# Optimization experiments

Hardware: AMD Instinct MI355X
Metric: run time of the kernel (lower is better)

## Reference

```python
import jax, jax.numpy as jnp
import numpy as np

N = 100000        # nodes
E = 3200000       # edges
IN = 256          # in_feats
H = 8             # num_heads
O = 64            # out_feats
F = 64            # edge_feats
T = 8             # num_etypes

def setup_inputs() -> dict:
    key = jax.random.key(0)
    ks = jax.random.split(key, 10)
    return {
        "feat": jax.random.normal(ks[0], (N, IN), jnp.float32) * 0.1,
        "etype": jax.random.randint(ks[1], (E,), 0, T, jnp.int32),
        "src": jax.random.randint(ks[2], (E,), 0, N, jnp.int32),
        "dst": jax.random.randint(ks[3], (E,), 0, N, jnp.int32),
        "W_fc": jax.random.normal(ks[4], (IN, H * O), jnp.float32) * (1.0 / np.sqrt(IN)),
        "edge_emb": jax.random.normal(ks[5], (T, F), jnp.float32),
        "W_e": jax.random.normal(ks[6], (F, H * F), jnp.float32) * (1.0 / np.sqrt(F)),
        "attn_l": jax.random.normal(ks[7], (H, O), jnp.float32) * 0.1,
        "attn_r": jax.random.normal(ks[8], (H, O), jnp.float32) * 0.1,
        "attn_e": jax.random.normal(ks[9], (H, F), jnp.float32) * 0.1,
    }

def reference(feat, etype, src, dst, W_fc, edge_emb, W_e, attn_l, attn_r, attn_e):
    n = feat.shape[0]
    # node projection + per-head attention logits
    h = (feat @ W_fc).reshape(n, H, O)                      # [N,H,O]
    el = jnp.einsum('nho,ho->nh', h, attn_l)                # [N,H]
    er = jnp.einsum('nho,ho->nh', h, attn_r)                # [N,H]
    # edge-type embedding -> projection -> logit (project the tiny table once, then gather)
    emb_proj = (edge_emb @ W_e).reshape(T, H, F)            # [T,H,F]
    ee = jnp.einsum('thf,hf->th', emb_proj, attn_e)[etype]  # [E,H]
    # u_add_v + edge bias, then ReLU (module's "leaky_relu" is nn.ReLU())
    e = jax.nn.relu(el[src] + er[dst] + ee)                 # [E,H]
    # segment softmax grouped by destination node
    m = jax.ops.segment_max(e, dst, num_segments=n)         # [N,H]
    ex = jnp.exp(e - m[dst])                                # [E,H]
    s = jax.ops.segment_sum(ex, dst, num_segments=n)        # [N,H]
    return ex / s[dst]                                      # [E,H]
```

## Files before the change

kernel.cpp:

```cpp
#include <hip/hip_runtime.h>
#include <math.h>

#define NN 100000
#define NE 3200000
#define INF_ 256
#define NH 8
#define OF 64
#define EF 64
#define NT 8

#define BSH 7
#define BNODES 128
#define NB 782
#define CAPB 4608
#define SPLIT 4
#define EPB 4096

static constexpr size_t WS_AT      = 0;
static constexpr size_t WS_EE      = 4096;
static constexpr size_t WS_EL      = 4160;
static constexpr size_t WS_ERS     = WS_EL + (size_t)NN * 8;
static constexpr size_t WS_CCNT    = WS_ERS + (size_t)NN * 16;
static constexpr size_t WS_PART    = WS_CCNT + NB + 2;

__global__ __launch_bounds__(256) void k_prep_A(const float* __restrict__ W_fc,
                                                const float* __restrict__ attn_l,
                                                const float* __restrict__ attn_r,
                                                float* __restrict__ At,
                                                unsigned* __restrict__ ccnt) {
    int t = blockIdx.x * 256 + threadIdx.x;
    if (t < NB) ccnt[t] = 0u;
    int c = t >> 8;
    int i = t & 255;
    int h = c & 7;
    const float* attn = (c < 8) ? attn_l : attn_r;
    const float* wrow = W_fc + (size_t)i * (NH * OF) + h * OF;
    const float* arow = attn + h * OF;
    float acc = 0.f;
#pragma unroll 8
    for (int o = 0; o < OF; ++o) acc += wrow[o] * arow[o];
    At[c * INF_ + i] = acc;
}

__global__ __launch_bounds__(512) void k_prep_ee(const float* __restrict__ edge_emb,
                                                 const float* __restrict__ W_e,
                                                 const float* __restrict__ attn_e,
                                                 float* __restrict__ ee_tab) {
    __shared__ float B[EF][NH];
    int t = threadIdx.x;
    int g = t >> 3, h = t & 7;
    const float* wrow = W_e + (size_t)g * (NH * EF) + h * EF;
    const float* arow = attn_e + h * EF;
    float acc = 0.f;
#pragma unroll 8
    for (int f = 0; f < EF; ++f) acc += wrow[f] * arow[f];
    B[g][h] = acc;
    __syncthreads();
    if (t < NT * NH) {
        int tt = t >> 3, hh = t & 7;
        float a = 0.f;
#pragma unroll 8
        for (int g2 = 0; g2 < EF; ++g2) a += edge_emb[tt * EF + g2] * B[g2][hh];
        ee_tab[tt * NH + hh] = a;
    }
}

__global__ __launch_bounds__(256) void k_node(const float* __restrict__ feat,
                                              const float* __restrict__ At,
                                              float* __restrict__ el,
                                              float* __restrict__ ers) {
    int n = blockIdx.x * 256 + threadIdx.x;
    if (n >= NN) return;
    const float4* f4 = (const float4*)(feat + (size_t)n * INF_);
    const float4* A4 = (const float4*)At;
    float acc[16];
#pragma unroll
    for (int c = 0; c < 16; ++c) acc[c] = 0.f;
    for (int iq = 0; iq < INF_ / 4; ++iq) {
        float4 f = f4[iq];
#pragma unroll
        for (int c = 0; c < 16; ++c) {
            float4 a = A4[c * 64 + iq];
            acc[c] += f.x * a.x + f.y * a.y + f.z * a.z + f.w * a.w;
        }
    }
    float4* e4 = (float4*)(el + (size_t)n * 8);
    e4[0] = make_float4(acc[0], acc[1], acc[2], acc[3]);
    e4[1] = make_float4(acc[4], acc[5], acc[6], acc[7]);
    float4* r4 = (float4*)(ers + (size_t)n * 16);
    r4[0] = make_float4(acc[8], acc[9], acc[10], acc[11]);
    r4[1] = make_float4(acc[12], acc[13], acc[14], acc[15]);
    r4[2] = make_float4(0.f, 0.f, 0.f, 0.f);
    r4[3] = make_float4(0.f, 0.f, 0.f, 0.f);
}

__global__ __launch_bounds__(256) void k_partition(const int* __restrict__ src,
                                                   const int* __restrict__ dst,
                                                   const int* __restrict__ etype,
                                                   unsigned* __restrict__ ccnt,
                                                   unsigned* __restrict__ part) {
    __shared__ unsigned hist[NB];
    __shared__ unsigned cursor[NB];
    int tid = threadIdx.x;
    size_t base = (size_t)blockIdx.x * EPB;
    unsigned long long rc[16];
    for (int i = tid; i < NB; i += 256) hist[i] = 0u;
    __syncthreads();
#pragma unroll
    for (int k = 0; k < 16; ++k) {
        size_t j = base + (size_t)k * 256 + tid;
        if (j < NE) {
            int dj = dst[j];
            rc[k] = (unsigned long long)(unsigned)src[j]
                  | ((unsigned long long)(unsigned)etype[j] << 17)
                  | ((unsigned long long)(unsigned)dj << 20);
            atomicAdd(&hist[dj >> BSH], 1u);
        } else rc[k] = ~0ull;
    }
    __syncthreads();
    for (int i = tid; i < NB; i += 256) {
        unsigned h = hist[i];
        cursor[i] = h ? atomicAdd(ccnt + i, h) : 0u;
    }
    __syncthreads();
#pragma unroll
    for (int k = 0; k < 16; ++k) {
        if (rc[k] == ~0ull) continue;
        int dj = (int)(rc[k] >> 20);
        int b = dj >> BSH;
        unsigned pos = atomicAdd(&cursor[b], 1u);
        if (pos < CAPB)
            part[(size_t)b * CAPB + pos] =
                (unsigned)(rc[k] & 0xFFFFFull) | ((unsigned)(dj & (BNODES - 1)) << 20);
    }
}

__global__ __launch_bounds__(256) void k_bucket_sum(const unsigned* __restrict__ part,
                                                    const unsigned* __restrict__ ccnt,
                                                    const float* __restrict__ el,
                                                    const float* __restrict__ ers,
                                                    const float* __restrict__ ee_tab,
                                                    float* __restrict__ ers_out) {
    __shared__ float sbin[BNODES * 9];
    int bs = blockIdx.x;
    int b = bs >> 2, c = bs & 3;
    int tid = threadIdx.x;
    int n0 = b << BSH;
    int nn = NN - n0; if (nn > BNODES) nn = BNODES;

    for (int i = tid; i < BNODES * 9; i += 256) sbin[i] = 0.f;
    __syncthreads();

    unsigned cnt = ccnt[b]; if (cnt > CAPB) cnt = CAPB;
    const unsigned* pp = part + (size_t)b * CAPB;
    for (unsigned e = (unsigned)(c * 256 + tid); e < cnt; e += 1024) {
        unsigned rec = pp[e];
        int sj = (int)(rec & 0x1FFFFu);
        int et = (int)((rec >> 17) & 7u);
        int dl = (int)((rec >> 20) & (BNODES - 1));
        const float4* el4 = (const float4*)(el + (size_t)sj * 8);
        const float4* E   = (const float4*)(ers + (size_t)(n0 + dl) * 16);
        const float4* ee4 = (const float4*)(ee_tab + et * NH);
        float4 la = el4[0], lb = el4[1];
        float4 ra = E[0],   rb = E[1];
        float4 ea = ee4[0], eb = ee4[1];
        float* sb = &sbin[dl * 9];
        atomicAdd(&sb[0], __expf(fmaxf(la.x + ra.x + ea.x, 0.f)));
        atomicAdd(&sb[1], __expf(fmaxf(la.y + ra.y + ea.y, 0.f)));
        atomicAdd(&sb[2], __expf(fmaxf(la.z + ra.z + ea.z, 0.f)));
        atomicAdd(&sb[3], __expf(fmaxf(la.w + ra.w + ea.w, 0.f)));
        atomicAdd(&sb[4], __expf(fmaxf(lb.x + rb.x + eb.x, 0.f)));
        atomicAdd(&sb[5], __expf(fmaxf(lb.y + rb.y + eb.y, 0.f)));
        atomicAdd(&sb[6], __expf(fmaxf(lb.z + rb.z + eb.z, 0.f)));
        atomicAdd(&sb[7], __expf(fmaxf(lb.w + rb.w + eb.w, 0.f)));
    }
    __syncthreads();
    for (int i = tid; i < nn * NH; i += 256) {
        int nl = i >> 3, hh = i & 7;
        atomicAdd(&ers_out[(size_t)(n0 + nl) * 16 + 8 + hh], sbin[nl * 9 + hh]);
    }
}

__global__ __launch_bounds__(256) void k_edge_out(const int* __restrict__ src,
                                                  const int* __restrict__ dst,
                                                  const int* __restrict__ etype,
                                                  const float* __restrict__ el,
                                                  const float* __restrict__ ers,
                                                  const float* __restrict__ ee_tab,
                                                  float* __restrict__ out) {
    int j = blockIdx.x * 256 + threadIdx.x;
    if (j >= NE) return;
    int sj = src[j], dj = dst[j], tj = etype[j];
    const float4* el4 = (const float4*)(el + (size_t)sj * 8);
    const float4* E   = (const float4*)(ers + (size_t)dj * 16);
    const float4* ee4 = (const float4*)(ee_tab + tj * NH);
    float4 l0 = el4[0], l1 = el4[1];
    float4 r0 = E[0], r1 = E[1];
    float4 s0 = E[2], s1 = E[3];
    float4 e0 = ee4[0], e1 = ee4[1];
    float4 o0, o1;
    o0.x = __expf(fmaxf(l0.x + r0.x + e0.x, 0.f)) / s0.x;
    o0.y = __expf(fmaxf(l0.y + r0.y + e0.y, 0.f)) / s0.y;
    o0.z = __expf(fmaxf(l0.z + r0.z + e0.z, 0.f)) / s0.z;
    o0.w = __expf(fmaxf(l0.w + r0.w + e0.w, 0.f)) / s0.w;
    o1.x = __expf(fmaxf(l1.x + r1.x + e1.x, 0.f)) / s1.x;
    o1.y = __expf(fmaxf(l1.y + r1.y + e1.y, 0.f)) / s1.y;
    o1.z = __expf(fmaxf(l1.z + r1.z + e1.z, 0.f)) / s1.z;
    o1.w = __expf(fmaxf(l1.w + r1.w + e1.w, 0.f)) / s1.w;
    float4* o4 = (float4*)(out + (size_t)j * NH);
    o4[0] = o0;
    o4[1] = o1;
}

extern "C" void kernel_launch(void* const* d_in, const int* in_sizes, int n_in,
                              void* d_out, int out_size, void* d_ws, size_t ws_size,
                              hipStream_t stream) {
    const float* feat     = (const float*)d_in[0];
    const int*   etype    = (const int*)d_in[1];
    const int*   src      = (const int*)d_in[2];
    const int*   dst      = (const int*)d_in[3];
    const float* W_fc     = (const float*)d_in[4];
    const float* edge_emb = (const float*)d_in[5];
    const float* W_e      = (const float*)d_in[6];
    const float* attn_l   = (const float*)d_in[7];
    const float* attn_r   = (const float*)d_in[8];
    const float* attn_e   = (const float*)d_in[9];

    float*    ws      = (float*)d_ws;
    float*    At      = ws + WS_AT;
    float*    ee_tab  = ws + WS_EE;
    float*    el      = ws + WS_EL;
    float*    ers     = ws + WS_ERS;
    unsigned* ccnt    = (unsigned*)(ws + WS_CCNT);
    unsigned* part    = (unsigned*)(ws + WS_PART);
    float*    out     = (float*)d_out;

    hipLaunchKernelGGL(k_prep_A, dim3(16), dim3(256), 0, stream, W_fc, attn_l, attn_r, At, ccnt);
    hipLaunchKernelGGL(k_prep_ee, dim3(1), dim3(512), 0, stream, edge_emb, W_e, attn_e, ee_tab);
    hipLaunchKernelGGL(k_node, dim3((NN + 255) / 256), dim3(256), 0, stream, feat, At, el, ers);
    hipLaunchKernelGGL(k_partition, dim3((NE + EPB - 1) / EPB), dim3(256), 0, stream,
                       src, dst, etype, ccnt, part);
    hipLaunchKernelGGL(k_bucket_sum, dim3(NB * SPLIT), dim3(256), 0, stream,
                       part, ccnt, el, ers, ee_tab, ers);
    hipLaunchKernelGGL(k_edge_out, dim3((NE + 255) / 256), dim3(256), 0, stream,
                       src, dst, etype, el, ers, ee_tab, out);
}
```

Measured before the change: 519.6 us.

## Merge prep kernels, use nontemporal loads/stores, double partition edges per block

Fuses the two tiny prep kernels into one 17-block launch to save a kernel launch. Streaming reads of feat, src/dst/etype and partition records, and the output writes, now use nontemporal builtins so they bypass cache retention. The partition kernel processes 8192 edges per block with 32 records held per thread, halving block count and global atomics on bucket counters at the cost of more registers and fewer blocks.

Result: slower. 543.8 us (+4.7%).

```diff
diff --git a/kernel.cpp b/kernel.cpp
--- a/kernel.cpp
+++ b/kernel.cpp
@@ -14,7 +14,9 @@
 #define NB 782
 #define CAPB 4608
 #define SPLIT 4
-#define EPB 4096
+#define EPB 8192
+
+typedef float vf4 __attribute__((ext_vector_type(4)));
 
 static constexpr size_t WS_AT      = 0;
 static constexpr size_t WS_EE      = 4096;
@@ -23,45 +25,50 @@
 static constexpr size_t WS_CCNT    = WS_ERS + (size_t)NN * 16;
 static constexpr size_t WS_PART    = WS_CCNT + NB + 2;
 
-__global__ __launch_bounds__(256) void k_prep_A(const float* __restrict__ W_fc,
-                                                const float* __restrict__ attn_l,
-                                                const float* __restrict__ attn_r,
-                                                float* __restrict__ At,
-                                                unsigned* __restrict__ ccnt) {
-    int t = blockIdx.x * 256 + threadIdx.x;
-    if (t < NB) ccnt[t] = 0u;
-    int c = t >> 8;
-    int i = t & 255;
-    int h = c & 7;
-    const float* attn = (c < 8) ? attn_l : attn_r;
-    const float* wrow = W_fc + (size_t)i * (NH * OF) + h * OF;
-    const float* arow = attn + h * OF;
-    float acc = 0.f;
+__global__ __launch_bounds__(256) void k_prep(const float* __restrict__ W_fc,
+                                              const float* __restrict__ attn_l,
+                                              const float* __restrict__ attn_r,
+                                              const float* __restrict__ edge_emb,
+                                              const float* __restrict__ W_e,
+                                              const float* __restrict__ attn_e,
+                                              float* __restrict__ At,
+                                              float* __restrict__ ee_tab,
+                                              unsigned* __restrict__ ccnt) {
+    if (blockIdx.x < 16) {
+        int t = blockIdx.x * 256 + threadIdx.x;
+        if (t < NB) ccnt[t] = 0u;
+        int c = t >> 8;
+        int i = t & 255;
+        int h = c & 7;
+        const float* attn = (c < 8) ? attn_l : attn_r;
+        const float* wrow = W_fc + (size_t)i * (NH * OF) + h * OF;
+        const float* arow = attn + h * OF;
+        float acc = 0.f;
 #pragma unroll 8
-    for (int o = 0; o < OF; ++o) acc += wrow[o] * arow[o];
-    At[c * INF_ + i] = acc;
-}
-
-__global__ __launch_bounds__(512) void k_prep_ee(const float* __restrict__ edge_emb,
-                                                 const float* __restrict__ W_e,
-                                                 const float* __restrict__ attn_e,
-                                                 float* __restrict__ ee_tab) {
-    __shared__ float B[EF][NH];
-    int t = threadIdx.x;
-    int g = t >> 3, h = t & 7;
-    const float* wrow = W_e + (size_t)g * (NH * EF) + h * EF;
-    const float* arow = attn_e + h * EF;
-    float acc = 0.f;
+        for (int o = 0; o < OF; ++o) acc += wrow[o] * arow[o];
+        At[c * INF_ + i] = acc;
+    } else {
+        __shared__ float B[EF][NH];
+        int t = threadIdx.x;
+#pragma unroll
+        for (int p = 0; p < 2; ++p) {
+            int idx = t + p * 256;
+            int g = idx >> 3, h = idx & 7;
+            const float* wrow = W_e + (size_t)g * (NH * EF) + h * EF;
+            const float* arow = attn_e + h * EF;
+            float acc = 0.f;
 #pragma unroll 8
-    for (int f = 0; f < EF; ++f) acc += wrow[f] * arow[f];
-    B[g][h] = acc;
-    __syncthreads();
-    if (t < NT * NH) {
-        int tt = t >> 3, hh = t & 7;
-        float a = 0.f;
+            for (int f = 0; f < EF; ++f) acc += wrow[f] * arow[f];
+            B[g][h] = acc;
+        }
+        __syncthreads();
+        if (t < NT * NH) {
+            int tt = t >> 3, hh = t & 7;
+            float a = 0.f;
 #pragma unroll 8
-        for (int g2 = 0; g2 < EF; ++g2) a += edge_emb[tt * EF + g2] * B[g2][hh];
-        ee_tab[tt * NH + hh] = a;
+            for (int g2 = 0; g2 < EF; ++g2) a += edge_emb[tt * EF + g2] * B[g2][hh];
+            ee_tab[tt * NH + hh] = a;
+        }
     }
 }
 
@@ -71,13 +78,13 @@
                                               float* __restrict__ ers) {
     int n = blockIdx.x * 256 + threadIdx.x;
     if (n >= NN) return;
-    const float4* f4 = (const float4*)(feat + (size_t)n * INF_);
+    const vf4* f4 = (const vf4*)(feat + (size_t)n * INF_);
     const float4* A4 = (const float4*)At;
     float acc[16];
 #pragma unroll
     for (int c = 0; c < 16; ++c) acc[c] = 0.f;
     for (int iq = 0; iq < INF_ / 4; ++iq) {
-        float4 f = f4[iq];
+        vf4 f = __builtin_nontemporal_load(f4 + iq);
 #pragma unroll
         for (int c = 0; c < 16; ++c) {
             float4 a = A4[c * 64 + iq];
@@ -103,16 +110,18 @@
     __shared__ unsigned cursor[NB];
     int tid = threadIdx.x;
     size_t base = (size_t)blockIdx.x * EPB;
-    unsigned long long rc[16];
+    unsigned long long rc[32];
     for (int i = tid; i < NB; i += 256) hist[i] = 0u;
     __syncthreads();
 #pragma unroll
-    for (int k = 0; k < 16; ++k) {
+    for (int k = 0; k < 32; ++k) {
         size_t j = base + (size_t)k * 256 + tid;
         if (j < NE) {
-            int dj = dst[j];
-            rc[k] = (unsigned long long)(unsigned)src[j]
-                  | ((unsigned long long)(unsigned)etype[j] << 17)
+            int dj = __builtin_nontemporal_load(dst + j);
+            int sj = __builtin_nontemporal_load(src + j);
+            int tj = __builtin_nontemporal_load(etype + j);
+            rc[k] = (unsigned long long)(unsigned)sj
+                  | ((unsigned long long)(unsigned)tj << 17)
                   | ((unsigned long long)(unsigned)dj << 20);
             atomicAdd(&hist[dj >> BSH], 1u);
         } else rc[k] = ~0ull;
@@ -124,7 +133,7 @@
     }
     __syncthreads();
 #pragma unroll
-    for (int k = 0; k < 16; ++k) {
+    for (int k = 0; k < 32; ++k) {
         if (rc[k] == ~0ull) continue;
         int dj = (int)(rc[k] >> 20);
         int b = dj >> BSH;
@@ -154,7 +163,7 @@
     unsigned cnt = ccnt[b]; if (cnt > CAPB) cnt = CAPB;
     const unsigned* pp = part + (size_t)b * CAPB;
     for (unsigned e = (unsigned)(c * 256 + tid); e < cnt; e += 1024) {
-        unsigned rec = pp[e];
+        unsigned rec = __builtin_nontemporal_load(pp + e);
         int sj = (int)(rec & 0x1FFFFu);
         int et = (int)((rec >> 17) & 7u);
         int dl = (int)((rec >> 20) & (BNODES - 1));
@@ -190,7 +199,9 @@
                                                   float* __restrict__ out) {
     int j = blockIdx.x * 256 + threadIdx.x;
     if (j >= NE) return;
-    int sj = src[j], dj = dst[j], tj = etype[j];
+    int sj = __builtin_nontemporal_load(src + j);
+    int dj = __builtin_nontemporal_load(dst + j);
+    int tj = __builtin_nontemporal_load(etype + j);
     const float4* el4 = (const float4*)(el + (size_t)sj * 8);
     const float4* E   = (const float4*)(ers + (size_t)dj * 16);
     const float4* ee4 = (const float4*)(ee_tab + tj * NH);
@@ -198,7 +209,7 @@
     float4 r0 = E[0], r1 = E[1];
     float4 s0 = E[2], s1 = E[3];
     float4 e0 = ee4[0], e1 = ee4[1];
-    float4 o0, o1;
+    vf4 o0, o1;
     o0.x = __expf(fmaxf(l0.x + r0.x + e0.x, 0.f)) / s0.x;
     o0.y = __expf(fmaxf(l0.y + r0.y + e0.y, 0.f)) / s0.y;
     o0.z = __expf(fmaxf(l0.z + r0.z + e0.z, 0.f)) / s0.z;
@@ -207,9 +218,9 @@
     o1.y = __expf(fmaxf(l1.y + r1.y + e1.y, 0.f)) / s1.y;
     o1.z = __expf(fmaxf(l1.z + r1.z + e1.z, 0.f)) / s1.z;
     o1.w = __expf(fmaxf(l1.w + r1.w + e1.w, 0.f)) / s1.w;
-    float4* o4 = (float4*)(out + (size_t)j * NH);
-    o4[0] = o0;
-    o4[1] = o1;
+    vf4* o4 = (vf4*)(out + (size_t)j * NH);
+    __builtin_nontemporal_store(o0, o4);
+    __builtin_nontemporal_store(o1, o4 + 1);
 }
 
 extern "C" void kernel_launch(void* const* d_in, const int* in_sizes, int n_in,
@@ -235,8 +246,8 @@
     unsigned* part    = (unsigned*)(ws + WS_PART);
     float*    out     = (float*)d_out;
 
-    hipLaunchKernelGGL(k_prep_A, dim3(16), dim3(256), 0, stream, W_fc, attn_l, attn_r, At, ccnt);
-    hipLaunchKernelGGL(k_prep_ee, dim3(1), dim3(512), 0, stream, edge_emb, W_e, attn_e, ee_tab);
+    hipLaunchKernelGGL(k_prep, dim3(17), dim3(256), 0, stream,
+                       W_fc, attn_l, attn_r, edge_emb, W_e, attn_e, At, ee_tab, ccnt);
     hipLaunchKernelGGL(k_node, dim3((NN + 255) / 256), dim3(256), 0, stream, feat, At, el, ers);
     hipLaunchKernelGGL(k_partition, dim3((NE + EPB - 1) / EPB), dim3(256), 0, stream,
                        src, dst, etype, ccnt, part);
```
